# Kernel tuning notes

Hardware: AMD Instinct MI355X
Metric: run time of the kernel (lower is better)

Reference implementation:

```python
import jax, jax.numpy as jnp
import numpy as np

N_NODES = 50000
N_EDGES = 800000
D_IN = 128
D_HID = 128
D_OUT = 128


def setup_inputs() -> dict:
    key = jax.random.key(0)
    ks = jax.random.split(key, 10)
    x = jax.random.normal(ks[0], (N_NODES, D_IN), dtype=jnp.float32)
    edge_index = jax.random.randint(ks[1], (2, N_EDGES), 0, N_NODES, dtype=jnp.int64)
    edge_index_inter = jax.random.randint(ks[2], (2, N_EDGES), 0, N_NODES, dtype=jnp.int64)
    # nn.Linear-style params: W [out, in], b [out]
    def linear(k, fan_in, fan_out):
        k1, k2 = jax.random.split(k)
        bound = 1.0 / np.sqrt(fan_in)
        W = jax.random.uniform(k1, (fan_out, fan_in), minval=-bound, maxval=bound, dtype=jnp.float32)
        b = jax.random.uniform(k2, (fan_out,), minval=-bound, maxval=bound, dtype=jnp.float32)
        return W, b
    W1, b1 = linear(ks[3], D_IN, D_HID)
    W2, b2 = linear(ks[4], D_HID, D_HID)
    W3, b3 = linear(ks[5], D_HID, D_OUT)
    return {"x": x, "W1": W1, "b1": b1, "W2": W2, "b2": b2, "W3": W3, "b3": b3,
            "edge_index": edge_index, "edge_index_inter": edge_index_inter}


def _gnn_layer(h, W, b, src, dst, n_nodes):
    # message: lin(x_j - x_i); x_j = source features, x_i = target features (PyG convention)
    msg = (h[src] - h[dst]) @ W.T + b          # [E, out]
    # aggr='add': scatter-add messages into target nodes
    return jax.ops.segment_sum(msg, dst, num_segments=n_nodes)  # [N, out]


def reference(x, W1, b1, W2, b2, W3, b3, edge_index, edge_index_inter):
    src, dst = edge_index[0], edge_index[1]
    n = x.shape[0]
    h = _gnn_layer(x, W1, b1, src, dst, n)
    h = _gnn_layer(h, W2, b2, src, dst, n)
    return _gnn_layer(h, W3, b3, src, dst, n)
```

## Files before the change

kernel.cpp:

```cpp
#include <hip/hip_runtime.h>

#define N_NODES 50000
#define N_EDGES 800000
#define D 128
#define TN 16
#define TSTR 136
#define SCAN_BLOCKS 196

typedef __attribute__((ext_vector_type(8))) short bf16x8;
typedef __attribute__((ext_vector_type(4))) float f32x4;

__device__ __forceinline__ unsigned short f32_to_bf16_rne(float f) {
    unsigned u = __float_as_uint(f);
    u += 0x7fffu + ((u >> 16) & 1u);
    return (unsigned short)(u >> 16);
}

__device__ __forceinline__ void acc_bf16x4(uint2 r, float& x, float& y, float& z, float& w) {
    x += __uint_as_float(r.x << 16);
    y += __uint_as_float(r.x & 0xffff0000u);
    z += __uint_as_float(r.y << 16);
    w += __uint_as_float(r.y & 0xffff0000u);
}

template <int U>
__device__ __forceinline__ void gather_phase(const unsigned short* __restrict__ hb,
                                             int myidx, int i, int sub, int q,
                                             float* ax, float* ay, float* az, float* aw) {
    int si[U];
    uint2 rr[U];
#pragma unroll
    for (int u = 0; u < U; ++u) si[u] = __shfl(myidx, i + 2 * u + sub, 64);
#pragma unroll
    for (int u = 0; u < U; ++u) rr[u] = *(const uint2*)(hb + (size_t)si[u] * D + 4 * q);
#pragma unroll
    for (int u = 0; u < U; ++u)
        acc_bf16x4(rr[u], ax[u & 3], ay[u & 3], az[u & 3], aw[u & 3]);
}

__global__ void prep_kernel(const int* __restrict__ dst, int* __restrict__ counts,
                            unsigned short* __restrict__ rank,
                            const float* __restrict__ x, unsigned short* __restrict__ xb) {
    const int t = blockIdx.x * blockDim.x + threadIdx.x;
    if (t < N_EDGES) {
        rank[t] = (unsigned short)atomicAdd(&counts[dst[t]], 1);
    }
    {
        const float4 v0 = *(const float4*)(x + (size_t)t * 8);
        const float4 v1 = *(const float4*)(x + (size_t)t * 8 + 4);
        uint4 p;
        p.x = (unsigned)f32_to_bf16_rne(v0.x) | ((unsigned)f32_to_bf16_rne(v0.y) << 16);
        p.y = (unsigned)f32_to_bf16_rne(v0.z) | ((unsigned)f32_to_bf16_rne(v0.w) << 16);
        p.z = (unsigned)f32_to_bf16_rne(v1.x) | ((unsigned)f32_to_bf16_rne(v1.y) << 16);
        p.w = (unsigned)f32_to_bf16_rne(v1.z) | ((unsigned)f32_to_bf16_rne(v1.w) << 16);
        *(uint4*)(xb + (size_t)t * 8) = p;
    }
}

__global__ void block_sum_kernel(const int* __restrict__ counts, int* __restrict__ bsum) {
    __shared__ int red[256];
    const int tid = threadIdx.x;
    const int i = blockIdx.x * 256 + tid;
    red[tid] = (i < N_NODES) ? counts[i] : 0;
    __syncthreads();
    for (int s = 128; s > 0; s >>= 1) {
        if (tid < s) red[tid] += red[tid + s];
        __syncthreads();
    }
    if (tid == 0) bsum[blockIdx.x] = red[0];
}

__global__ void bsum_scan_kernel(const int* __restrict__ bsum,
                                 int* __restrict__ bpre,
                                 int* __restrict__ offsets) {
    __shared__ int s[256];
    const int tid = threadIdx.x;
    const int v = (tid < SCAN_BLOCKS) ? bsum[tid] : 0;
    s[tid] = v;
    __syncthreads();
    for (int off = 1; off < 256; off <<= 1) {
        int a = (tid >= off) ? s[tid - off] : 0;
        __syncthreads();
        s[tid] += a;
        __syncthreads();
    }
    bpre[tid] = s[tid] - v;
    if (tid == 255) offsets[N_NODES] = s[255];
}

__global__ void offsets_wfrag_kernel(const int* __restrict__ counts,
                                     const int* __restrict__ bpre,
                                     int* __restrict__ offsets,
                                     const float* __restrict__ W1,
                                     const float* __restrict__ W2,
                                     const float* __restrict__ W3,
                                     unsigned short* __restrict__ Wb) {
    if (blockIdx.x < SCAN_BLOCKS) {
        __shared__ int s[256];
        const int tid = threadIdx.x;
        const int i = blockIdx.x * 256 + tid;
        const int v = (i < N_NODES) ? counts[i] : 0;
        s[tid] = v;
        __syncthreads();
        for (int off = 1; off < 256; off <<= 1) {
            int a = (tid >= off) ? s[tid - off] : 0;
            __syncthreads();
            s[tid] += a;
            __syncthreads();
        }
        const int excl = s[tid] - v + bpre[blockIdx.x];
        if (i < N_NODES) offsets[i] = excl;
    } else {
        const int unit = (blockIdx.x - SCAN_BLOCKS) * 2 + (threadIdx.x >> 7);
        const int w = unit >> 7;
        const int o = unit & 127;
        const int k = threadIdx.x & 127;
        const float* W = (w == 0) ? W1 : (w == 1) ? W2 : W3;
        const unsigned short v = f32_to_bf16_rne(W[o * D + k]);
        const int nt = o >> 4, n = o & 15;
        const int kc = k >> 5, kr = k & 31, quad = kr >> 3, j = kr & 7;
        const int lane = quad * 16 + n;
        Wb[(((size_t)w * 8 + nt) * 4 + kc) * 512 + lane * 8 + j] = v;
    }
}

__global__ void fill_kernel(const int* __restrict__ src, const int* __restrict__ dst,
                            const unsigned short* __restrict__ rank,
                            const int* __restrict__ offsets,
                            unsigned short* __restrict__ esrc) {
    int e = blockIdx.x * blockDim.x + threadIdx.x;
    if (e < N_EDGES) {
        esrc[offsets[dst[e]] + (int)rank[e]] = (unsigned short)src[e];
    }
}

template <bool OUT_BF16>
__global__ __launch_bounds__(256) void gnn_layer_kernel(
    const unsigned short* __restrict__ hb,
    const int* __restrict__ offsets,
    const unsigned short* __restrict__ esrc,
    const unsigned short* __restrict__ Wb,
    const float* __restrict__ bias,
    float* __restrict__ outf,
    unsigned short* __restrict__ outb) {

    __shared__ __align__(16) unsigned short tb[TN][TSTR];
    __shared__ float degf[TN];

    const int tid = threadIdx.x;
    const int wave = tid >> 6;
    const int lane = tid & 63;
    const int sub = lane >> 5;
    const int q = lane & 31;
    const int vbase = blockIdx.x * TN;

    for (int j = wave * 4; j < wave * 4 + 4; ++j) {
        const int v = vbase + j;
        const int beg = offsets[v];
        const int deg = offsets[v + 1] - beg;

        float ax[4] = {0.f, 0.f, 0.f, 0.f};
        float ay[4] = {0.f, 0.f, 0.f, 0.f};
        float az[4] = {0.f, 0.f, 0.f, 0.f};
        float aw[4] = {0.f, 0.f, 0.f, 0.f};

        for (int base = 0; base < deg; base += 64) {
            const int cnt = min(deg - base, 64);
            int myidx = 0;
            if (lane < cnt) myidx = (int)esrc[beg + base + lane];

            int i = 0;
            for (; i + 16 <= cnt; i += 16)
                gather_phase<8>(hb, myidx, i, sub, q, ax, ay, az, aw);
            if (i + 8 <= cnt) {
                gather_phase<4>(hb, myidx, i, sub, q, ax, ay, az, aw);
                i += 8;
            }
            if (i + 4 <= cnt) {
                gather_phase<2>(hb, myidx, i, sub, q, ax, ay, az, aw);
                i += 4;
            }
            if (i + 2 <= cnt) {
                gather_phase<1>(hb, myidx, i, sub, q, ax, ay, az, aw);
                i += 2;
            }
            if (i < cnt) {
                const int s0 = __shfl(myidx, i, 64);
                if (sub == 0) {
                    const uint2 r = *(const uint2*)(hb + (size_t)s0 * D + 4 * q);
                    acc_bf16x4(r, ax[0], ay[0], az[0], aw[0]);
                }
            }
        }

        float sx = (ax[0] + ax[1]) + (ax[2] + ax[3]);
        float sy = (ay[0] + ay[1]) + (ay[2] + ay[3]);
        float sz = (az[0] + az[1]) + (az[2] + az[3]);
        float sw = (aw[0] + aw[1]) + (aw[2] + aw[3]);

        sx += __shfl_xor(sx, 32, 64);
        sy += __shfl_xor(sy, 32, 64);
        sz += __shfl_xor(sz, 32, 64);
        sw += __shfl_xor(sw, 32, 64);

        const float dv = (float)deg;
        if (sub == 0) {
            const uint2 r = *(const uint2*)(hb + (size_t)v * D + 4 * q);
            const float tx = sx - dv * __uint_as_float(r.x << 16);
            const float ty = sy - dv * __uint_as_float(r.x & 0xffff0000u);
            const float tz = sz - dv * __uint_as_float(r.y << 16);
            const float tw = sw - dv * __uint_as_float(r.y & 0xffff0000u);
            unsigned p0 = (unsigned)f32_to_bf16_rne(tx) | ((unsigned)f32_to_bf16_rne(ty) << 16);
            unsigned p1 = (unsigned)f32_to_bf16_rne(tz) | ((unsigned)f32_to_bf16_rne(tw) << 16);
            *(uint2*)&tb[j][4 * q] = make_uint2(p0, p1);
        }
        if (lane == 0) degf[j] = dv;
    }
    __syncthreads();

    const int n16 = lane & 15;
    const int quad = lane >> 4;

    bf16x8 afrag[4];
#pragma unroll
    for (int kc = 0; kc < 4; ++kc)
        afrag[kc] = *(const bf16x8*)&tb[n16][kc * 32 + quad * 8];

#pragma unroll
    for (int i = 0; i < 2; ++i) {
        const int nt = wave * 2 + i;
        f32x4 acc = {0.f, 0.f, 0.f, 0.f};
#pragma unroll
        for (int kc = 0; kc < 4; ++kc) {
            const bf16x8 bfrag = *(const bf16x8*)&Wb[((nt * 4 + kc) * 64 + lane) * 8];
            acc = __builtin_amdgcn_mfma_f32_16x16x32_bf16(afrag[kc], bfrag, acc, 0, 0, 0);
        }
        const int o = nt * 16 + n16;
        const float bo = bias[o];
#pragma unroll
        for (int r = 0; r < 4; ++r) {
            const int m = quad * 4 + r;
            const float val = acc[r] + degf[m] * bo;
            if (OUT_BF16)
                outb[(size_t)(vbase + m) * D + o] = f32_to_bf16_rne(val);
            else
                outf[(size_t)(vbase + m) * D + o] = val;
        }
    }
}

extern "C" void kernel_launch(void* const* d_in, const int* in_sizes, int n_in,
                              void* d_out, int out_size, void* d_ws, size_t ws_size,
                              hipStream_t stream) {
    const float* x  = (const float*)d_in[0];
    const float* W1 = (const float*)d_in[1];
    const float* b1 = (const float*)d_in[2];
    const float* W2 = (const float*)d_in[3];
    const float* b2 = (const float*)d_in[4];
    const float* W3 = (const float*)d_in[5];
    const float* b3 = (const float*)d_in[6];
    const int*   ei = (const int*)d_in[7];

    const int* src = ei;
    const int* dst = ei + N_EDGES;
    float* out = (float*)d_out;

    char* ws = (char*)d_ws;
    int* counts  = (int*)ws;                          ws += 204800;
    int* offsets = (int*)ws;                          ws += 204800;
    int* bsum    = (int*)ws;                          ws += 1024;
    int* bpre    = (int*)ws;                          ws += 1024;
    unsigned short* rank = (unsigned short*)ws;       ws += (size_t)N_EDGES * 2;
    unsigned short* esrc = (unsigned short*)ws;       ws += (size_t)N_EDGES * 2;
    unsigned short* Wb = (unsigned short*)ws;         ws += 3 * 16384 * 2;
    unsigned short* xb = (unsigned short*)ws;         ws += (size_t)N_NODES * D * 2;
    unsigned short* h1 = (unsigned short*)ws;         ws += (size_t)N_NODES * D * 2;
    unsigned short* h2 = (unsigned short*)ws;

    hipMemsetAsync(counts, 0, N_NODES * sizeof(int), stream);
    prep_kernel<<<(N_EDGES + 255) / 256, 256, 0, stream>>>(dst, counts, rank, x, xb);
    block_sum_kernel<<<SCAN_BLOCKS, 256, 0, stream>>>(counts, bsum);
    bsum_scan_kernel<<<1, 256, 0, stream>>>(bsum, bpre, offsets);
    offsets_wfrag_kernel<<<SCAN_BLOCKS + 192, 256, 0, stream>>>(counts, bpre, offsets,
                                                                W1, W2, W3, Wb);
    fill_kernel<<<(N_EDGES + 255) / 256, 256, 0, stream>>>(src, dst, rank, offsets, esrc);

    const int blocks = N_NODES / TN;

    gnn_layer_kernel<true ><<<blocks, 256, 0, stream>>>(xb, offsets, esrc, Wb,          b1, nullptr, h1);
    gnn_layer_kernel<true ><<<blocks, 256, 0, stream>>>(h1, offsets, esrc, Wb + 16384,  b2, nullptr, h2);
    gnn_layer_kernel<false><<<blocks, 256, 0, stream>>>(h2, offsets, esrc, Wb + 32768,  b3, out, nullptr);
}
```

Measured before the change: 265.3 us.

## Split each wave into half-waves gathering nodes with 16-byte row loads

The gather stage now gives each 32-lane half-wave its own pair of destination nodes. Each 16-lane group loads a full 256-byte neighbor row as uint4 (8 bf16 per lane), so two neighbor rows are fetched per half-wave step instead of one row per 32 lanes with 8-byte loads. The goal is wider memory transactions and more independent nodes in flight per wave, to hide gather latency. The cost is more accumulator registers (16 floats per node) and load imbalance within a wave when the nodes have different degrees.

```diff
diff --git a/kernel.cpp b/kernel.cpp
--- a/kernel.cpp
+++ b/kernel.cpp
@@ -16,26 +16,64 @@
     return (unsigned short)(u >> 16);
 }
 
-__device__ __forceinline__ void acc_bf16x4(uint2 r, float& x, float& y, float& z, float& w) {
-    x += __uint_as_float(r.x << 16);
-    y += __uint_as_float(r.x & 0xffff0000u);
-    z += __uint_as_float(r.y << 16);
-    w += __uint_as_float(r.y & 0xffff0000u);
+__device__ __forceinline__ float bflo(unsigned u) { return __uint_as_float(u << 16); }
+__device__ __forceinline__ float bfhi(unsigned u) { return __uint_as_float(u & 0xffff0000u); }
+
+__device__ __forceinline__ void acc8(uint4 r, float* a) {
+    a[0] += bflo(r.x); a[1] += bfhi(r.x);
+    a[2] += bflo(r.y); a[3] += bfhi(r.y);
+    a[4] += bflo(r.z); a[5] += bfhi(r.z);
+    a[6] += bflo(r.w); a[7] += bfhi(r.w);
 }
 
 template <int U>
-__device__ __forceinline__ void gather_phase(const unsigned short* __restrict__ hb,
-                                             int myidx, int i, int sub, int q,
-                                             float* ax, float* ay, float* az, float* aw) {
+__device__ __forceinline__ void gather16(const unsigned short* __restrict__ hb,
+                                         int myidx, int i, int rowid2, int d8,
+                                         float* a0, float* a1) {
     int si[U];
-    uint2 rr[U];
-#pragma unroll
-    for (int u = 0; u < U; ++u) si[u] = __shfl(myidx, i + 2 * u + sub, 64);
-#pragma unroll
-    for (int u = 0; u < U; ++u) rr[u] = *(const uint2*)(hb + (size_t)si[u] * D + 4 * q);
-#pragma unroll
-    for (int u = 0; u < U; ++u)
-        acc_bf16x4(rr[u], ax[u & 3], ay[u & 3], az[u & 3], aw[u & 3]);
+    uint4 rr[U];
+#pragma unroll
+    for (int u = 0; u < U; ++u) si[u] = __shfl(myidx, i + 2 * u + rowid2, 32);
+#pragma unroll
+    for (int u = 0; u < U; ++u) rr[u] = *(const uint4*)(hb + (size_t)si[u] * D + 8 * d8);
+#pragma unroll
+    for (int u = 0; u < U; ++u) acc8(rr[u], (u & 1) ? a1 : a0);
+}
+
+__device__ __forceinline__ void gather_node(const unsigned short* __restrict__ hb,
+                                            const unsigned short* __restrict__ esrc,
+                                            int beg, int deg, int idx0,
+                                            int l32, int rowid2, int d8,
+                                            float* out) {
+    float a0[8] = {0.f, 0.f, 0.f, 0.f, 0.f, 0.f, 0.f, 0.f};
+    float a1[8] = {0.f, 0.f, 0.f, 0.f, 0.f, 0.f, 0.f, 0.f};
+    int myidx = idx0;
+    int base = 0;
+    while (true) {
+        const int cnt = min(deg - base, 32);
+        int i = 0;
+        for (; i + 16 <= cnt; i += 16) gather16<8>(hb, myidx, i, rowid2, d8, a0, a1);
+        if (i + 8 <= cnt) { gather16<4>(hb, myidx, i, rowid2, d8, a0, a1); i += 8; }
+        if (i + 4 <= cnt) { gather16<2>(hb, myidx, i, rowid2, d8, a0, a1); i += 4; }
+        if (i + 2 <= cnt) { gather16<1>(hb, myidx, i, rowid2, d8, a0, a1); i += 2; }
+        if (i < cnt) {
+            const int s0 = __shfl(myidx, i, 32);
+            if (rowid2 == 0) {
+                const uint4 r = *(const uint4*)(hb + (size_t)s0 * D + 8 * d8);
+                acc8(r, a0);
+            }
+        }
+        base += 32;
+        if (base >= deg) break;
+        myidx = 0;
+        if (l32 < deg - base) myidx = (int)esrc[beg + base + l32];
+    }
+#pragma unroll
+    for (int k = 0; k < 8; ++k) {
+        float s = a0[k] + a1[k];
+        s += __shfl_xor(s, 16, 64);
+        out[k] = s;
+    }
 }
 
 __global__ void prep_kernel(const int* __restrict__ dst, int* __restrict__ counts,
@@ -150,71 +188,46 @@
     const int tid = threadIdx.x;
     const int wave = tid >> 6;
     const int lane = tid & 63;
-    const int sub = lane >> 5;
-    const int q = lane & 31;
+    const int half = lane >> 5;
+    const int l32 = lane & 31;
+    const int rowid2 = (lane >> 4) & 1;
+    const int d8 = lane & 15;
     const int vbase = blockIdx.x * TN;
 
-    for (int j = wave * 4; j < wave * 4 + 4; ++j) {
-        const int v = vbase + j;
-        const int beg = offsets[v];
-        const int deg = offsets[v + 1] - beg;
-
-        float ax[4] = {0.f, 0.f, 0.f, 0.f};
-        float ay[4] = {0.f, 0.f, 0.f, 0.f};
-        float az[4] = {0.f, 0.f, 0.f, 0.f};
-        float aw[4] = {0.f, 0.f, 0.f, 0.f};
-
-        for (int base = 0; base < deg; base += 64) {
-            const int cnt = min(deg - base, 64);
-            int myidx = 0;
-            if (lane < cnt) myidx = (int)esrc[beg + base + lane];
-
-            int i = 0;
-            for (; i + 16 <= cnt; i += 16)
-                gather_phase<8>(hb, myidx, i, sub, q, ax, ay, az, aw);
-            if (i + 8 <= cnt) {
-                gather_phase<4>(hb, myidx, i, sub, q, ax, ay, az, aw);
-                i += 8;
-            }
-            if (i + 4 <= cnt) {
-                gather_phase<2>(hb, myidx, i, sub, q, ax, ay, az, aw);
-                i += 4;
-            }
-            if (i + 2 <= cnt) {
-                gather_phase<1>(hb, myidx, i, sub, q, ax, ay, az, aw);
-                i += 2;
-            }
-            if (i < cnt) {
-                const int s0 = __shfl(myidx, i, 64);
-                if (sub == 0) {
-                    const uint2 r = *(const uint2*)(hb + (size_t)s0 * D + 4 * q);
-                    acc_bf16x4(r, ax[0], ay[0], az[0], aw[0]);
-                }
-            }
-        }
-
-        float sx = (ax[0] + ax[1]) + (ax[2] + ax[3]);
-        float sy = (ay[0] + ay[1]) + (ay[2] + ay[3]);
-        float sz = (az[0] + az[1]) + (az[2] + az[3]);
-        float sw = (aw[0] + aw[1]) + (aw[2] + aw[3]);
-
-        sx += __shfl_xor(sx, 32, 64);
-        sy += __shfl_xor(sy, 32, 64);
-        sz += __shfl_xor(sz, 32, 64);
-        sw += __shfl_xor(sw, 32, 64);
-
-        const float dv = (float)deg;
-        if (sub == 0) {
-            const uint2 r = *(const uint2*)(hb + (size_t)v * D + 4 * q);
-            const float tx = sx - dv * __uint_as_float(r.x << 16);
-            const float ty = sy - dv * __uint_as_float(r.x & 0xffff0000u);
-            const float tz = sz - dv * __uint_as_float(r.y << 16);
-            const float tw = sw - dv * __uint_as_float(r.y & 0xffff0000u);
-            unsigned p0 = (unsigned)f32_to_bf16_rne(tx) | ((unsigned)f32_to_bf16_rne(ty) << 16);
-            unsigned p1 = (unsigned)f32_to_bf16_rne(tz) | ((unsigned)f32_to_bf16_rne(tw) << 16);
-            *(uint2*)&tb[j][4 * q] = make_uint2(p0, p1);
-        }
-        if (lane == 0) degf[j] = dv;
+    const int j0 = wave * 4 + half * 2;
+    const int v0 = vbase + j0;
+
+    const int begA = offsets[v0];
+    const int begB = offsets[v0 + 1];
+    const int degA = begB - begA;
+    const int degB = offsets[v0 + 2] - begB;
+
+    int idxA = 0, idxB = 0;
+    if (l32 < min(degA, 32)) idxA = (int)esrc[begA + l32];
+    if (l32 < min(degB, 32)) idxB = (int)esrc[begB + l32];
+
+    float sA[8], sB[8];
+    gather_node(hb, esrc, begA, degA, idxA, l32, rowid2, d8, sA);
+    gather_node(hb, esrc, begB, degB, idxB, l32, rowid2, d8, sB);
+
+    {
+        const int vv = v0 + rowid2;
+        const float dv = (float)(rowid2 ? degB : degA);
+        const uint4 r = *(const uint4*)(hb + (size_t)vv * D + 8 * d8);
+        float t[8];
+#pragma unroll
+        for (int k = 0; k < 8; ++k) t[k] = rowid2 ? sB[k] : sA[k];
+        t[0] -= dv * bflo(r.x); t[1] -= dv * bfhi(r.x);
+        t[2] -= dv * bflo(r.y); t[3] -= dv * bfhi(r.y);
+        t[4] -= dv * bflo(r.z); t[5] -= dv * bfhi(r.z);
+        t[6] -= dv * bflo(r.w); t[7] -= dv * bfhi(r.w);
+        uint4 p;
+        p.x = (unsigned)f32_to_bf16_rne(t[0]) | ((unsigned)f32_to_bf16_rne(t[1]) << 16);
+        p.y = (unsigned)f32_to_bf16_rne(t[2]) | ((unsigned)f32_to_bf16_rne(t[3]) << 16);
+        p.z = (unsigned)f32_to_bf16_rne(t[4]) | ((unsigned)f32_to_bf16_rne(t[5]) << 16);
+        p.w = (unsigned)f32_to_bf16_rne(t[6]) | ((unsigned)f32_to_bf16_rne(t[7]) << 16);
+        *(uint4*)&tb[j0 + rowid2][8 * d8] = p;
+        if (d8 == 0) degf[j0 + rowid2] = dv;
     }
     __syncthreads();
 
```

Result: faster. 252.7 us (-4.8%).
